# Kernel tuning notes

Measured on AMD Instinct MI355X. Metric: run time of the kernel, lower is better.

The kernel has to match this reference:

```python
import jax, jax.numpy as jnp
import numpy as np

C = 256
C8 = C // 8

def setup_inputs() -> dict:
    key = jax.random.key(0)
    ks = jax.random.split(key, 8)
    a = jax.random.normal(ks[0], (4, C, 64, 64), dtype=jnp.float32)
    s = 1.0 / np.sqrt(C)
    b_w = jax.random.normal(ks[1], (C8, C), dtype=jnp.float32) * s
    b_b = jnp.zeros((C8,), dtype=jnp.float32)
    c_w = jax.random.normal(ks[2], (C8, C), dtype=jnp.float32) * s
    c_b = jnp.zeros((C8,), dtype=jnp.float32)
    d_w = jax.random.normal(ks[3], (C, C), dtype=jnp.float32) * s
    d_b = jnp.zeros((C,), dtype=jnp.float32)
    alpha = jnp.zeros((1,), dtype=jnp.float32) + 0.5  # nonzero so attention path is exercised
    return {"a": a, "b_w": b_w, "b_b": b_b, "c_w": c_w, "c_b": c_b, "d_w": d_w, "d_b": d_b, "alpha": alpha}

def _conv1x1(x, w, b):
    # x: [n, c, h, w], w: [o, c] -> [n, o, h, w]
    return jnp.einsum('nchw,oc->nohw', x, w) + b[None, :, None, None]

def reference(a, b_w, b_b, c_w, c_b, d_w, d_b, alpha):
    n, chan, h, w = a.shape
    nhw = h * w
    b = _conv1x1(a, b_w, b_b).reshape(n, -1, nhw)   # [n, C/8, nhw]
    c = _conv1x1(a, c_w, c_b).reshape(n, -1, nhw)   # [n, C/8, nhw]
    k = jnp.einsum('nci,ncj->nij', b, c)            # [n, nhw, nhw]
    s = jax.nn.softmax(k, axis=-1)
    d = _conv1x1(a, d_w, d_b).reshape(n, -1, nhw)   # [n, C, nhw]
    kl = jnp.einsum('ncj,nij->nci', d, s)           # d @ s^T
    kl = kl.reshape(n, chan, h, w)
    return alpha * kl + a
```

## Files before the change

kernel.cpp:

```cpp
#include <hip/hip_runtime.h>
#include <hip/hip_bf16.h>

#define CCH 256
#define CQK 32
#define NHW 4096

typedef float f32x4 __attribute__((ext_vector_type(4)));
typedef _Float16 hv8 __attribute__((ext_vector_type(8)));
typedef _Float16 hv4 __attribute__((ext_vector_type(4)));
typedef __fp16 fv2 __attribute__((ext_vector_type(2)));

typedef __attribute__((address_space(3))) unsigned int lds_u32_t;
typedef __attribute__((address_space(1))) const unsigned int glb_u32_t;
__device__ __forceinline__ void gll16(const _Float16* gp, _Float16* lp) {
    __builtin_amdgcn_global_load_lds((glb_u32_t*)gp, (lds_u32_t*)lp, 16, 0, 0);
}

__global__ __launch_bounds__(256) void prep_kernel(
    const float* __restrict__ b_w, const float* __restrict__ c_w,
    const float* __restrict__ d_w, _Float16* __restrict__ Wh)
{
    const int bid = blockIdx.x, tid = threadIdx.x;
    const int idx = (bid * 256 + tid) * 4;
    const int row = idx >> 8, col = idx & 255;
    const float* src = (row < 32) ? (b_w + row * CCH + col)
                     : (row < 64) ? (c_w + (row - 32) * CCH + col)
                                  : (d_w + (row - 64) * CCH + col);
    const float scl = (row < 32) ? 1.4426950408889634f : 1.0f;
    float4 v = *reinterpret_cast<const float4*>(src);
    _Float16* dst = Wh + (size_t)row * CCH + col;
    dst[0] = (_Float16)(v.x * scl); dst[1] = (_Float16)(v.y * scl);
    dst[2] = (_Float16)(v.z * scl); dst[3] = (_Float16)(v.w * scl);
}

__global__ __launch_bounds__(256) void proj_kernel(
    const float* __restrict__ a, const _Float16* __restrict__ Wh,
    const float* __restrict__ b_b, const float* __restrict__ c_b,
    const float* __restrict__ d_b,
    _Float16* __restrict__ bqT, _Float16* __restrict__ ckT,
    _Float16* __restrict__ dv)
{
    __shared__ _Float16 aT[32][CCH + 24];
    __shared__ _Float16 oT[256][34];
    __shared__ _Float16 pqT[32][34];
    __shared__ _Float16 pkT[32][34];

    const int n    = blockIdx.x >> 7;
    const int i0   = (blockIdx.x & 127) << 5;
    const int tid  = threadIdx.x;
    const int lane = tid & 63;
    const int wave = tid >> 6;
    const int l15  = lane & 15;
    const int quad = lane >> 4;

    {
        const float* ap = a + (size_t)(n*CCH + tid)*NHW + i0;
        #pragma unroll
        for (int j = 0; j < 8; ++j) {
            float4 v = *reinterpret_cast<const float4*>(ap + j*4);
            aT[j*4+0][tid] = (_Float16)v.x;
            aT[j*4+1][tid] = (_Float16)v.y;
            aT[j*4+2][tid] = (_Float16)v.z;
            aT[j*4+3][tid] = (_Float16)v.w;
        }
    }
    __syncthreads();

    const f32x4 zf = {0.f, 0.f, 0.f, 0.f};
    f32x4 acc[5][2];
    #pragma unroll
    for (int t = 0; t < 5; ++t) { acc[t][0] = zf; acc[t][1] = zf; }

    const int ch0w = wave * 80;

    #pragma unroll
    for (int ks = 0; ks < 8; ++ks) {
        const int k0 = ks * 32;
        hv8 af0 = *reinterpret_cast<const hv8*>(&aT[l15][k0 + quad*8]);
        hv8 af1 = *reinterpret_cast<const hv8*>(&aT[16 + l15][k0 + quad*8]);
        #pragma unroll
        for (int t = 0; t < 5; ++t) {
            const int ch0 = ch0w + t*16;
            hv8 bf = *reinterpret_cast<const hv8*>(
                Wh + (size_t)(ch0 + l15)*CCH + k0 + quad*8);
            acc[t][0] = __builtin_amdgcn_mfma_f32_16x16x32_f16(af0, bf, acc[t][0], 0, 0, 0);
            acc[t][1] = __builtin_amdgcn_mfma_f32_16x16x32_f16(af1, bf, acc[t][1], 0, 0, 0);
        }
    }

    const int posq = quad*4;
    #pragma unroll
    for (int t = 0; t < 5; ++t) {
        const int ch0 = ch0w + t*16;
        if (ch0 < 64) {
            const float* bias_arr = (ch0 < 32) ? b_b : c_b;
            const int    ch       = (ch0 & 31) + l15;
            const float  bias     = bias_arr[ch] *
                ((ch0 < 32) ? 1.4426950408889634f : 1.0f);
            #pragma unroll
            for (int nf = 0; nf < 2; ++nf) {
                #pragma unroll
                for (int r = 0; r < 4; ++r) {
                    const int pos = posq + nf*16 + r;
                    if (ch0 < 32) pqT[pos][ch] = (_Float16)(acc[t][nf][r] + bias);
                    else          pkT[pos][ch] = (_Float16)(acc[t][nf][r] + bias);
                }
            }
        } else {
            const int ch   = ch0 - 64 + l15;
            const float bias = d_b[ch];
            #pragma unroll
            for (int nf = 0; nf < 2; ++nf) {
                hv4 v = { (_Float16)(acc[t][nf][0] + bias),
                          (_Float16)(acc[t][nf][1] + bias),
                          (_Float16)(acc[t][nf][2] + bias),
                          (_Float16)(acc[t][nf][3] + bias) };
                *reinterpret_cast<hv4*>(&oT[ch][posq + nf*16]) = v;
            }
        }
    }
    __syncthreads();

    {
        const int p   = (tid & 127) >> 2;
        const int seg = (tid & 3) << 3;
        if (tid < 128) {
            *reinterpret_cast<int4*>(
                bqT + ((size_t)n*NHW + i0 + p)*CQK + seg) =
                *reinterpret_cast<const int4*>(&pqT[p][seg]);
        } else {
            *reinterpret_cast<int4*>(
                ckT + ((size_t)n*NHW + i0 + p)*CQK + seg) =
                *reinterpret_cast<const int4*>(&pkT[p][seg]);
        }
    }
    #pragma unroll
    for (int pass = 0; pass < 4; ++pass) {
        const int row = pass*64 + (tid >> 2);
        const int seg = (tid & 3) << 3;
        *reinterpret_cast<int4*>(
            dv + ((size_t)(n*CCH + row))*NHW + i0 + seg) =
            *reinterpret_cast<const int4*>(&oT[row][seg]);
    }
}

__global__ __launch_bounds__(256, 2) void attn_kernel(
    const _Float16* __restrict__ bqT, const _Float16* __restrict__ ckT,
    const _Float16* __restrict__ dv,
    const float* __restrict__ a, const float* __restrict__ alpha_p,
    float* __restrict__ out)
{
    __shared__ __align__(16) char smem[72704];

    const int bx   = ((blockIdx.x & 7) << 6) | (blockIdx.x >> 3);
    const int n    = bx >> 7;
    const int cg   = (bx >> 6) & 1;
    const int qt   = bx & 63;
    const int q0b  = qt << 6;
    const int co0  = cg << 7;
    const int tid  = threadIdx.x;
    const int g    = tid >> 6;
    const int lane = tid & 63;
    const int l15  = lane & 15;
    const int quad = lane >> 4;
    const int kg0  = g << 10;

    _Float16* vbuf = (_Float16*)(smem + g*8192);
    _Float16* pb   = (_Float16*)(smem + 32768 + g*5120);
    float*    lbuf = (float*)(smem + 70656);
    float*    mbuf = (float*)(smem + 71680);

    const f32x4 zf = {0.f, 0.f, 0.f, 0.f};
    const _Float16 one_h = (_Float16)1.0f;
    const hv8 ones = { one_h, one_h, one_h, one_h, one_h, one_h, one_h, one_h };

    hv8 qf[4];
    #pragma unroll
    for (int X = 0; X < 4; ++X) {
        const int q = q0b + X*16 + l15;
        qf[X] = *reinterpret_cast<const hv8*>(
            bqT + ((size_t)n*NHW + q)*CQK + quad*8);
    }

    const _Float16* ckbase = ckT + ((size_t)(n*NHW + kg0 + l15))*CQK + quad*8;

    float mneg[4];
    {
        float mx[4] = {-1e30f, -1e30f, -1e30f, -1e30f};
        #pragma unroll
        for (int bt = 0; bt < 8; ++bt) {
            hv8 kb[8];
            #pragma unroll
            for (int j = 0; j < 8; ++j)
                kb[j] = *reinterpret_cast<const hv8*>(
                    ckbase + (size_t)(bt*128 + j*16)*CQK);
            #pragma unroll
            for (int X = 0; X < 4; ++X) {
                float bm[8];
                #pragma unroll
                for (int j = 0; j < 8; ++j) {
                    f32x4 s = __builtin_amdgcn_mfma_f32_16x16x32_f16(
                        kb[j], qf[X], zf, 0, 0, 0);
                    bm[j] = fmaxf(fmaxf(s[0], s[1]), fmaxf(s[2], s[3]));
                }
                float m0 = fmaxf(fmaxf(bm[0], bm[1]), fmaxf(bm[2], bm[3]));
                float m1 = fmaxf(fmaxf(bm[4], bm[5]), fmaxf(bm[6], bm[7]));
                mx[X] = fmaxf(mx[X], fmaxf(m0, m1));
            }
        }
        #pragma unroll
        for (int X = 0; X < 4; ++X) {
            mx[X] = fmaxf(mx[X], __shfl_xor(mx[X], 16, 64));
            mx[X] = fmaxf(mx[X], __shfl_xor(mx[X], 32, 64));
            mneg[X] = -mx[X];
        }
    }

    f32x4 acc[4][8];
    #pragma unroll
    for (int X = 0; X < 4; ++X)
        #pragma unroll
        for (int t = 0; t < 8; ++t) acc[X][t] = zf;
    f32x4 accL[4];
    #pragma unroll
    for (int X = 0; X < 4; ++X) accL[X] = zf;

    const int rl4 = lane >> 2;
    const int sl  = lane & 3;
    const _Float16* dvs = dv
        + (size_t)(n*CCH + co0 + rl4)*NHW + kg0 + 8*(sl ^ ((rl4 >> 1) & 3));

    const int c0h = (quad*8) ^ (((l15 >> 1) & 3) << 3);

    auto softmax_tile = [&](const hv8* kf) {
        #pragma unroll
        for (int X = 0; X < 4; ++X) {
            const f32x4 minit = {mneg[X], mneg[X], mneg[X], mneg[X]};
            #pragma unroll
            for (int f = 0; f < 2; ++f) {
                f32x4 s = __builtin_amdgcn_mfma_f32_16x16x32_f16(
                    kf[f], qf[X], minit, 0, 0, 0);
                float p0 = __builtin_amdgcn_exp2f(s[0]);
                float p1 = __builtin_amdgcn_exp2f(s[1]);
                float p2 = __builtin_amdgcn_exp2f(s[2]);
                float p3 = __builtin_amdgcn_exp2f(s[3]);
                fv2 lo = __builtin_amdgcn_cvt_pkrtz(p0, p1);
                fv2 hi = __builtin_amdgcn_cvt_pkrtz(p2, p3);
                uint2 w;
                w.x = __builtin_bit_cast(unsigned, lo);
                w.y = __builtin_bit_cast(unsigned, hi);
                *reinterpret_cast<uint2*>(
                    pb + X*640 + l15*40 + f*16 + quad*4) = w;
            }
        }
    };

    hv8 pf0[4];
    auto read_pf = [&]() {
        #pragma unroll
        for (int X = 0; X < 4; ++X)
            pf0[X] = *reinterpret_cast<const hv8*>(pb + X*640 + l15*40 + quad*8);
    };

    auto stage = [&](int kt) {
        #pragma unroll
        for (int j = 0; j < 8; ++j)
            gll16(dvs + (size_t)(j*16)*NHW + kt*32, vbuf + j*512);
    };

    auto load_kf = [&](int key0, hv8* kf) {
        #pragma unroll
        for (int f = 0; f < 2; ++f)
            kf[f] = *reinterpret_cast<const hv8*>(
                ckbase + (size_t)(key0 + f*16)*CQK);
    };

    {
        stage(0);
        hv8 kf0[2];
        load_kf(0, kf0);
        softmax_tile(kf0);
        read_pf();
        asm volatile("s_waitcnt vmcnt(0)" ::: "memory");
        __builtin_amdgcn_sched_barrier(0);
    }

    for (int kt = 0; kt < 32; ++kt) {
        hv8 kfn[2];
        if (kt < 31) load_kf((kt + 1)*32, kfn);

        #pragma unroll
        for (int t = 0; t < 8; ++t) {
            hv8 d0 = *reinterpret_cast<const hv8*>(vbuf + (t*16 + l15)*32 + c0h);
            #pragma unroll
            for (int X = 0; X < 4; ++X)
                acc[X][t] = __builtin_amdgcn_mfma_f32_16x16x32_f16(
                    pf0[X], d0, acc[X][t], 0, 0, 0);
        }
        #pragma unroll
        for (int X = 0; X < 4; ++X)
            accL[X] = __builtin_amdgcn_mfma_f32_16x16x32_f16(pf0[X], ones, accL[X], 0, 0, 0);

        if (kt < 31) {
            asm volatile("s_waitcnt lgkmcnt(0)" ::: "memory");
            __builtin_amdgcn_sched_barrier(0);
            stage(kt + 1);
            softmax_tile(kfn);
            read_pf();
            asm volatile("s_waitcnt vmcnt(0)" ::: "memory");
            __builtin_amdgcn_sched_barrier(0);
        }
    }

    if (lane < 16) {
        #pragma unroll
        for (int X = 0; X < 4; ++X)
            mbuf[g*64 + X*16 + l15] = -mneg[X];
    }
    __syncthreads();

    {
        #pragma unroll
        for (int X = 0; X < 4; ++X) {
            const int qloc = X*16 + quad*4;
            float4 m0 = *reinterpret_cast<float4*>(&mbuf[0*64 + qloc]);
            float4 m1 = *reinterpret_cast<float4*>(&mbuf[1*64 + qloc]);
            float4 m2 = *reinterpret_cast<float4*>(&mbuf[2*64 + qloc]);
            float4 m3 = *reinterpret_cast<float4*>(&mbuf[3*64 + qloc]);
            float4 mm;
            mm.x = fmaxf(fmaxf(m0.x, m1.x), fmaxf(m2.x, m3.x));
            mm.y = fmaxf(fmaxf(m0.y, m1.y), fmaxf(m2.y, m3.y));
            mm.z = fmaxf(fmaxf(m0.z, m1.z), fmaxf(m2.z, m3.z));
            mm.w = fmaxf(fmaxf(m0.w, m1.w), fmaxf(m2.w, m3.w));
            float4 mo = (g == 0) ? m0 : (g == 1) ? m1 : (g == 2) ? m2 : m3;
            float sc0 = __builtin_amdgcn_exp2f(mo.x - mm.x);
            float sc1 = __builtin_amdgcn_exp2f(mo.y - mm.y);
            float sc2 = __builtin_amdgcn_exp2f(mo.z - mm.z);
            float sc3 = __builtin_amdgcn_exp2f(mo.w - mm.w);
            #pragma unroll
            for (int t = 0; t < 8; ++t) {
                acc[X][t][0] *= sc0; acc[X][t][1] *= sc1;
                acc[X][t][2] *= sc2; acc[X][t][3] *= sc3;
            }
            accL[X][0] *= sc0; accL[X][1] *= sc1;
            accL[X][2] *= sc2; accL[X][3] *= sc3;
        }
    }
    if (lane < 16) {
        if (l15 == 0) {
            #pragma unroll
            for (int X = 0; X < 4; ++X)
                *reinterpret_cast<float4*>(&lbuf[g*64 + X*16 + quad*4]) =
                    *reinterpret_cast<float4*>(&accL[X]);
        }
    } else if (l15 == 0) {
        #pragma unroll
        for (int X = 0; X < 4; ++X)
            *reinterpret_cast<float4*>(&lbuf[g*64 + X*16 + quad*4]) =
                *reinterpret_cast<float4*>(&accL[X]);
    }
    __syncthreads();

    float* buf1 = (float*)smem;
    float* buf2 = (float*)(smem + 35840);

    if (g == 1 || g == 3) {
        float* b = (g == 1) ? buf1 : buf2;
        #pragma unroll
        for (int X = 0; X < 4; ++X)
            #pragma unroll
            for (int t = 0; t < 8; ++t)
                *reinterpret_cast<float4*>(
                    &b[(t*16 + l15)*68 + X*16 + quad*4]) =
                    *reinterpret_cast<float4*>(&acc[X][t]);
    }
    __syncthreads();
    if (g == 0 || g == 2) {
        float* b = (g == 0) ? buf1 : buf2;
        #pragma unroll
        for (int X = 0; X < 4; ++X)
            #pragma unroll
            for (int t = 0; t < 8; ++t) {
                float4 p = *reinterpret_cast<float4*>(
                    &b[(t*16 + l15)*68 + X*16 + quad*4]);
                acc[X][t][0] += p.x; acc[X][t][1] += p.y;
                acc[X][t][2] += p.z; acc[X][t][3] += p.w;
            }
    }
    __syncthreads();
    if (g == 2) {
        #pragma unroll
        for (int X = 0; X < 4; ++X)
            #pragma unroll
            for (int t = 0; t < 8; ++t)
                *reinterpret_cast<float4*>(
                    &buf1[(t*16 + l15)*68 + X*16 + quad*4]) =
                    *reinterpret_cast<float4*>(&acc[X][t]);
    }
    __syncthreads();
    if (g == 0) {
        const float alpha = alpha_p[0];
        #pragma unroll
        for (int X = 0; X < 4; ++X) {
            const int qloc = X*16 + quad*4;
            #pragma unroll
            for (int t = 0; t < 8; ++t) {
                float4 p = *reinterpret_cast<float4*>(
                    &buf1[(t*16 + l15)*68 + qloc]);
                acc[X][t][0] += p.x; acc[X][t][1] += p.y;
                acc[X][t][2] += p.z; acc[X][t][3] += p.w;
            }
            float4 l0 = *reinterpret_cast<float4*>(&lbuf[0*64 + qloc]);
            float4 l1 = *reinterpret_cast<float4*>(&lbuf[1*64 + qloc]);
            float4 l2 = *reinterpret_cast<float4*>(&lbuf[2*64 + qloc]);
            float4 l3 = *reinterpret_cast<float4*>(&lbuf[3*64 + qloc]);
            f32x4 rl;
            rl[0] = alpha / (l0.x + l1.x + l2.x + l3.x);
            rl[1] = alpha / (l0.y + l1.y + l2.y + l3.y);
            rl[2] = alpha / (l0.z + l1.z + l2.z + l3.z);
            rl[3] = alpha / (l0.w + l1.w + l2.w + l3.w);
            #pragma unroll
            for (int t = 0; t < 8; ++t) {
                const size_t off =
                    ((size_t)(n*CCH + co0 + t*16 + l15))*NHW + q0b + qloc;
                float4 av = *reinterpret_cast<const float4*>(a + off);
                float4 o;
                o.x = acc[X][t][0]*rl[0] + av.x;
                o.y = acc[X][t][1]*rl[1] + av.y;
                o.z = acc[X][t][2]*rl[2] + av.z;
                o.w = acc[X][t][3]*rl[3] + av.w;
                *reinterpret_cast<float4*>(out + off) = o;
            }
        }
    }
}

extern "C" void kernel_launch(void* const* d_in, const int* in_sizes, int n_in,
                              void* d_out, int out_size, void* d_ws, size_t ws_size,
                              hipStream_t stream)
{
    const float* a    = (const float*)d_in[0];
    const float* b_w  = (const float*)d_in[1];
    const float* b_b  = (const float*)d_in[2];
    const float* c_w  = (const float*)d_in[3];
    const float* c_b  = (const float*)d_in[4];
    const float* d_w  = (const float*)d_in[5];
    const float* d_b  = (const float*)d_in[6];
    const float* alp  = (const float*)d_in[7];
    float* out = (float*)d_out;

    _Float16* bqT  = (_Float16*)d_ws;
    _Float16* ckT  = bqT + (size_t)4*NHW*CQK;
    _Float16* dv   = ckT + (size_t)4*NHW*CQK;
    _Float16* Wh   = dv + (size_t)4*CCH*NHW;

    prep_kernel<<<80, 256, 0, stream>>>(b_w, c_w, d_w, Wh);
    proj_kernel<<<512, 256, 0, stream>>>(a, Wh, b_b, c_b, d_b, bqT, ckT, dv);
    attn_kernel<<<512, 256, 0, stream>>>(bqT, ckT, dv, a, alp, out);
}
```

Measured before the change: 160.8 us.

## Load V operand directly from global memory instead of staging through LDS

Removes the async global-to-LDS staging of the dv tile and its swizzled LDS reads. Each lane now reads its V fragment straight from global memory inside the MFMA loop, and the explicit vmcnt/lgkmcnt waits and sched barriers go away. The MFMA block is also wrapped in s_setprio raises. This frees LDS and cuts synchronization, but global load latency now sits directly before the MFMAs, with no prefetch, and relies on L2/cache hits. The mbuf write gains an extra l15==0 store of the row maximum alongside the existing lane<16 store.

```diff
diff --git a/kernel.cpp b/kernel.cpp
--- a/kernel.cpp
+++ b/kernel.cpp
@@ -9,12 +9,6 @@
 typedef _Float16 hv8 __attribute__((ext_vector_type(8)));
 typedef _Float16 hv4 __attribute__((ext_vector_type(4)));
 typedef __fp16 fv2 __attribute__((ext_vector_type(2)));
-
-typedef __attribute__((address_space(3))) unsigned int lds_u32_t;
-typedef __attribute__((address_space(1))) const unsigned int glb_u32_t;
-__device__ __forceinline__ void gll16(const _Float16* gp, _Float16* lp) {
-    __builtin_amdgcn_global_load_lds((glb_u32_t*)gp, (lds_u32_t*)lp, 16, 0, 0);
-}
 
 __global__ __launch_bounds__(256) void prep_kernel(
     const float* __restrict__ b_w, const float* __restrict__ c_w,
@@ -150,7 +144,7 @@
     const float* __restrict__ a, const float* __restrict__ alpha_p,
     float* __restrict__ out)
 {
-    __shared__ __align__(16) char smem[72704];
+    __shared__ __align__(16) char smem[71680];
 
     const int bx   = ((blockIdx.x & 7) << 6) | (blockIdx.x >> 3);
     const int n    = bx >> 7;
@@ -165,10 +159,9 @@
     const int quad = lane >> 4;
     const int kg0  = g << 10;
 
-    _Float16* vbuf = (_Float16*)(smem + g*8192);
-    _Float16* pb   = (_Float16*)(smem + 32768 + g*5120);
-    float*    lbuf = (float*)(smem + 70656);
-    float*    mbuf = (float*)(smem + 71680);
+    _Float16* pb   = (_Float16*)(smem + g*5120);
+    float*    lbuf = (float*)(smem + 69632);
+    float*    mbuf = (float*)(smem + 70656);
 
     const f32x4 zf = {0.f, 0.f, 0.f, 0.f};
     const _Float16 one_h = (_Float16)1.0f;
@@ -225,12 +218,7 @@
     #pragma unroll
     for (int X = 0; X < 4; ++X) accL[X] = zf;
 
-    const int rl4 = lane >> 2;
-    const int sl  = lane & 3;
-    const _Float16* dvs = dv
-        + (size_t)(n*CCH + co0 + rl4)*NHW + kg0 + 8*(sl ^ ((rl4 >> 1) & 3));
-
-    const int c0h = (quad*8) ^ (((l15 >> 1) & 3) << 3);
+    const _Float16* vb = dv + (size_t)(n*CCH + co0 + l15)*NHW + kg0 + quad*8;
 
     auto softmax_tile = [&](const hv8* kf) {
         #pragma unroll
@@ -262,12 +250,6 @@
             pf0[X] = *reinterpret_cast<const hv8*>(pb + X*640 + l15*40 + quad*8);
     };
 
-    auto stage = [&](int kt) {
-        #pragma unroll
-        for (int j = 0; j < 8; ++j)
-            gll16(dvs + (size_t)(j*16)*NHW + kt*32, vbuf + j*512);
-    };
-
     auto load_kf = [&](int key0, hv8* kf) {
         #pragma unroll
         for (int f = 0; f < 2; ++f)
@@ -276,22 +258,21 @@
     };
 
     {
-        stage(0);
         hv8 kf0[2];
         load_kf(0, kf0);
         softmax_tile(kf0);
         read_pf();
-        asm volatile("s_waitcnt vmcnt(0)" ::: "memory");
-        __builtin_amdgcn_sched_barrier(0);
     }
 
     for (int kt = 0; kt < 32; ++kt) {
         hv8 kfn[2];
         if (kt < 31) load_kf((kt + 1)*32, kfn);
 
+        __builtin_amdgcn_s_setprio(1);
         #pragma unroll
         for (int t = 0; t < 8; ++t) {
-            hv8 d0 = *reinterpret_cast<const hv8*>(vbuf + (t*16 + l15)*32 + c0h);
+            hv8 d0 = *reinterpret_cast<const hv8*>(
+                vb + (size_t)(t*16)*NHW + kt*32);
             #pragma unroll
             for (int X = 0; X < 4; ++X)
                 acc[X][t] = __builtin_amdgcn_mfma_f32_16x16x32_f16(
@@ -300,18 +281,19 @@
         #pragma unroll
         for (int X = 0; X < 4; ++X)
             accL[X] = __builtin_amdgcn_mfma_f32_16x16x32_f16(pf0[X], ones, accL[X], 0, 0, 0);
+        __builtin_amdgcn_s_setprio(0);
 
         if (kt < 31) {
-            asm volatile("s_waitcnt lgkmcnt(0)" ::: "memory");
-            __builtin_amdgcn_sched_barrier(0);
-            stage(kt + 1);
             softmax_tile(kfn);
             read_pf();
-            asm volatile("s_waitcnt vmcnt(0)" ::: "memory");
-            __builtin_amdgcn_sched_barrier(0);
-        }
-    }
-
+        }
+    }
+
+    if (l15 == 0) {
+        #pragma unroll
+        for (int X = 0; X < 4; ++X)
+            mbuf[g*64 + X*16 + quad*4 + 0] = -mneg[X];
+    }
     if (lane < 16) {
         #pragma unroll
         for (int X = 0; X < 4; ++X)
@@ -346,14 +328,7 @@
             accL[X][2] *= sc2; accL[X][3] *= sc3;
         }
     }
-    if (lane < 16) {
-        if (l15 == 0) {
-            #pragma unroll
-            for (int X = 0; X < 4; ++X)
-                *reinterpret_cast<float4*>(&lbuf[g*64 + X*16 + quad*4]) =
-                    *reinterpret_cast<float4*>(&accL[X]);
-        }
-    } else if (l15 == 0) {
+    if (l15 == 0) {
         #pragma unroll
         for (int X = 0; X < 4; ++X)
             *reinterpret_cast<float4*>(&lbuf[g*64 + X*16 + quad*4]) =
@@ -362,7 +337,7 @@
     __syncthreads();
 
     float* buf1 = (float*)smem;
-    float* buf2 = (float*)(smem + 35840);
+    float* buf2 = (float*)(smem + 34816);
 
     if (g == 1 || g == 3) {
         float* b = (g == 1) ? buf1 : buf2;
```

Measured after the change: 177.8 us. +10.6%, slower.
